# Kernel tuning notes

Hardware: AMD Instinct MI355X
Metric: run time of the kernel (lower is better)

## Reference

```python
import jax, jax.numpy as jnp
import numpy as np

B, S, E = 4, 4096, 1024
H = 16
D = E // H            # per-head dim (k_dim == v_dim == 64)
N_SAMPLE = 1024       # tokens kept per (batch, head)


def setup_inputs() -> dict:
    key = jax.random.key(0)
    ks = jax.random.split(key, 7)
    lim = float(np.sqrt(6.0 / (E + E)))  # xavier_uniform for square weight
    x = jax.random.normal(ks[0], (B, S, E), dtype=jnp.float32)
    Wq = jax.random.uniform(ks[1], (E, E), jnp.float32, -lim, lim)
    Wk = jax.random.uniform(ks[2], (E, E), jnp.float32, -lim, lim)
    Wv = jax.random.uniform(ks[3], (E, E), jnp.float32, -lim, lim)
    bq = jnp.zeros((E,), jnp.float32)
    bk = jnp.zeros((E,), jnp.float32)
    bv = jnp.zeros((E,), jnp.float32)
    return {"x": x, "Wq": Wq, "bq": bq, "Wk": Wk, "bk": bk, "Wv": Wv, "bv": bv}


def reference(x, Wq, bq, Wk, bk, Wv, bv):
    Bs, Sl, Ed = x.shape
    # projections -> [B, H, S, D]
    q = (x @ Wq.T + bq).reshape(Bs, Sl, H, D).transpose(0, 2, 1, 3)
    k = (x @ Wk.T + bk).reshape(Bs, Sl, H, D).transpose(0, 2, 1, 3)
    v = (x @ Wv.T + bv).reshape(Bs, Sl, H, D).transpose(0, 2, 1, 3)

    # cosFormer feature map: relu + cos/sin positional reweighting
    pos = jnp.arange(Sl, dtype=x.dtype)
    theta = (jnp.pi / 2.0) * pos / Sl            # [S]
    cos_w = jnp.cos(theta)[None, None, :, None]  # [1,1,S,1]
    sin_w = jnp.sin(theta)[None, None, :, None]
    qn = jax.nn.relu(q)
    kn = jax.nn.relu(k)
    q_cos, q_sin = qn * cos_w, qn * sin_w
    k_cos, k_sin = kn * cos_w, kn * sin_w

    # token sampler: top-N_SAMPLE tokens by (q*k).sum(-1) per (b,h)
    scores = jnp.sum(q * k, axis=-1)             # [B,H,S]
    _, idx = jax.lax.top_k(scores, N_SAMPLE)     # [B,H,n]

    # global K^T V reductions: [B,H,D,D]
    kv_cos = jnp.einsum("bhsd,bhse->bhde", k_cos, v)
    kv_sin = jnp.einsum("bhsd,bhse->bhde", k_sin, v)

    # gather sampled queries: [B,H,n,D]
    qs_cos = jnp.take_along_axis(q_cos, idx[..., None], axis=2)
    qs_sin = jnp.take_along_axis(q_sin, idx[..., None], axis=2)

    sampled = (jnp.einsum("bhnd,bhde->bhne", qs_cos, kv_cos)
               + jnp.einsum("bhnd,bhde->bhne", qs_sin, kv_sin))  # [B,H,n,D]

    # scatter-add back into zeros at sampled positions
    bi = jnp.arange(Bs)[:, None, None]
    hi = jnp.arange(H)[None, :, None]
    values = jnp.zeros((Bs, H, Sl, D), sampled.dtype).at[bi, hi, idx].add(sampled)

    out = values.transpose(0, 2, 1, 3).reshape(Bs, Sl, H * D)
    return out  # o_proj is Identity (v_dim*num_heads == embed_dim); dropout=0
```

## Files before the change

### kernel.cpp

```cpp
#include <hip/hip_runtime.h>
#include <hip/hip_bf16.h>

#define B_ 4
#define S_ 4096
#define E_ 1024
#define H_ 16
#define D_ 64
#define NS_ 1024
#define M_ (B_*S_)
#define K_ E_
#define DELTA 0.12f
#define BANDCAP 96

typedef __attribute__((ext_vector_type(8))) short bf16x8;
typedef __attribute__((ext_vector_type(4))) float floatx4;

#define THSTEP 0.00038349519697141023f

__device__ inline float bf16_to_f(unsigned short u) {
    return __uint_as_float(((unsigned)u) << 16);
}
__device__ inline unsigned short f_to_bf16(float f) {
    unsigned u = __float_as_uint(f);
    unsigned r = (u + 0x7FFFu + ((u >> 16) & 1u)) >> 16;
    return (unsigned short)r;
}

__device__ inline void gl_lds16(const void* g, void* l) {
    __builtin_amdgcn_global_load_lds(
        (const __attribute__((address_space(1))) void*)g,
        (__attribute__((address_space(3))) void*)l, 16, 0, 0);
}

__global__ __launch_bounds__(256) void split_x_kernel(
    const float* __restrict__ x, ushort* __restrict__ xh)
{
    int i = blockIdx.x * 256 + threadIdx.x;
    float4 v = ((const float4*)x)[i];
    ushort4 hh;
    hh.x = f_to_bf16(v.x); hh.y = f_to_bf16(v.y);
    hh.z = f_to_bf16(v.z); hh.w = f_to_bf16(v.w);
    ((ushort4*)xh)[i] = hh;
}

__global__ __launch_bounds__(256) void split_w_kernel(
    const float* __restrict__ Wq, const float* __restrict__ Wk,
    const float* __restrict__ Wv,
    ushort* __restrict__ Wqh, ushort* __restrict__ Wql,
    ushort* __restrict__ Wkh, ushort* __restrict__ Wkl,
    ushort* __restrict__ Wvh)
{
    int i = blockIdx.x * 256 + threadIdx.x;
    float4 q = ((const float4*)Wq)[i];
    float4 k = ((const float4*)Wk)[i];
    float4 v = ((const float4*)Wv)[i];
    ushort4 h, l;
    h.x=f_to_bf16(q.x); l.x=f_to_bf16(q.x-bf16_to_f(h.x));
    h.y=f_to_bf16(q.y); l.y=f_to_bf16(q.y-bf16_to_f(h.y));
    h.z=f_to_bf16(q.z); l.z=f_to_bf16(q.z-bf16_to_f(h.z));
    h.w=f_to_bf16(q.w); l.w=f_to_bf16(q.w-bf16_to_f(h.w));
    ((ushort4*)Wqh)[i]=h; ((ushort4*)Wql)[i]=l;
    h.x=f_to_bf16(k.x); l.x=f_to_bf16(k.x-bf16_to_f(h.x));
    h.y=f_to_bf16(k.y); l.y=f_to_bf16(k.y-bf16_to_f(h.y));
    h.z=f_to_bf16(k.z); l.z=f_to_bf16(k.z-bf16_to_f(h.z));
    h.w=f_to_bf16(k.w); l.w=f_to_bf16(k.w-bf16_to_f(h.w));
    ((ushort4*)Wkh)[i]=h; ((ushort4*)Wkl)[i]=l;
    h.x=f_to_bf16(v.x); h.y=f_to_bf16(v.y);
    h.z=f_to_bf16(v.z); h.w=f_to_bf16(v.w);
    ((ushort4*)Wvh)[i]=h;
}

__global__ __launch_bounds__(256) void qkv_gemm(
    const ushort* __restrict__ xh,
    const ushort* __restrict__ Wqh, const ushort* __restrict__ Wql,
    const ushort* __restrict__ Wkh, const ushort* __restrict__ Wkl,
    const ushort* __restrict__ Wvh,
    const float* __restrict__ bq, const float* __restrict__ bk,
    const float* __restrict__ bv,
    float* __restrict__ q32, float* __restrict__ k32, ushort* __restrict__ v16)
{
    __shared__ __align__(16) ushort As[128 * 64];
    __shared__ __align__(16) ushort Bsh[128 * 64];
    __shared__ __align__(16) ushort Bsl[128 * 64];

    const int w = blockIdx.z;
    const ushort* Bhp = (w == 0) ? Wqh : (w == 1) ? Wkh : Wvh;
    const ushort* Blp = (w == 0) ? Wql : Wkl;
    const float* bias = (w == 0) ? bq : (w == 1) ? bk : bv;
    const bool lo = (w < 2);

    const int m0 = blockIdx.x * 128;
    const int n0 = blockIdx.y * 128;
    const int t = threadIdx.x;
    const int wave = t >> 6, lane = t & 63;
    const int wm = (wave >> 1) * 64, wn = (wave & 1) * 64;
    const int m16 = lane & 15, quad = lane >> 4;

    floatx4 acc[4][4];
#pragma unroll
    for (int i = 0; i < 4; i++)
#pragma unroll
        for (int j = 0; j < 4; j++) acc[i][j] = (floatx4){0.f, 0.f, 0.f, 0.f};

    int aoff[4], boff[4], lbase[4];
#pragma unroll
    for (int i = 0; i < 4; i++) {
        int slot = i * 256 + t;
        int r = slot >> 3, c = slot & 7, g = c ^ (r & 7);
        aoff[i] = (m0 + r) * K_ + g * 8;
        boff[i] = (n0 + r) * K_ + g * 8;
        lbase[i] = (i * 256 + wave * 64) * 8;
    }

    for (int ks = 0; ks < 16; ++ks) {
        const int kcol = ks * 64;
#pragma unroll
        for (int i = 0; i < 4; i++) {
            gl_lds16(xh + aoff[i] + kcol, &As[lbase[i]]);
            gl_lds16(Bhp + boff[i] + kcol, &Bsh[lbase[i]]);
        }
        if (lo) {
#pragma unroll
            for (int i = 0; i < 4; i++)
                gl_lds16(Blp + boff[i] + kcol, &Bsl[lbase[i]]);
        }
        __syncthreads();

#pragma unroll
        for (int kk = 0; kk < 2; ++kk) {
            bf16x8 af[4], bfr[4];
            const int g = kk * 4 + quad;
#pragma unroll
            for (int mt = 0; mt < 4; ++mt) {
                int r = wm + mt * 16 + m16;
                af[mt] = *(const bf16x8*)&As[(r * 8 + (g ^ (r & 7))) * 8];
            }
#pragma unroll
            for (int nt = 0; nt < 4; ++nt) {
                int r2 = wn + nt * 16 + m16;
                bfr[nt] = *(const bf16x8*)&Bsh[(r2 * 8 + (g ^ (r2 & 7))) * 8];
            }
#pragma unroll
            for (int mt = 0; mt < 4; ++mt)
#pragma unroll
                for (int nt = 0; nt < 4; ++nt)
                    acc[mt][nt] = __builtin_amdgcn_mfma_f32_16x16x32_bf16(
                        af[mt], bfr[nt], acc[mt][nt], 0, 0, 0);
            if (lo) {
#pragma unroll
                for (int nt = 0; nt < 4; ++nt) {
                    int r2 = wn + nt * 16 + m16;
                    bfr[nt] = *(const bf16x8*)&Bsl[(r2 * 8 + (g ^ (r2 & 7))) * 8];
                }
#pragma unroll
                for (int mt = 0; mt < 4; ++mt)
#pragma unroll
                    for (int nt = 0; nt < 4; ++nt)
                        acc[mt][nt] = __builtin_amdgcn_mfma_f32_16x16x32_bf16(
                            af[mt], bfr[nt], acc[mt][nt], 0, 0, 0);
            }
        }
        __syncthreads();
    }

    float biasv[4];
#pragma unroll
    for (int nt = 0; nt < 4; nt++)
        biasv[nt] = bias[n0 + wn + nt * 16 + m16];

    if (w < 2) {
        float* dst = (w == 0) ? q32 : k32;
#pragma unroll
        for (int mt = 0; mt < 4; ++mt)
#pragma unroll
            for (int nt = 0; nt < 4; ++nt) {
                int colg = n0 + wn + nt * 16 + m16;
#pragma unroll
                for (int reg = 0; reg < 4; ++reg) {
                    int rowg = m0 + wm + mt * 16 + quad * 4 + reg;
                    dst[(size_t)rowg * E_ + colg] = acc[mt][nt][reg] + biasv[nt];
                }
            }
    } else {
#pragma unroll
        for (int mt = 0; mt < 4; ++mt)
#pragma unroll
            for (int nt = 0; nt < 4; ++nt) {
                int colg = n0 + wn + nt * 16 + m16;
#pragma unroll
                for (int reg = 0; reg < 4; ++reg) {
                    int rowg = m0 + wm + mt * 16 + quad * 4 + reg;
                    v16[(size_t)rowg * E_ + colg] = f_to_bf16(acc[mt][nt][reg] + biasv[nt]);
                }
            }
    }
}

__global__ __launch_bounds__(256) void scores_kernel(
    const float* __restrict__ q32, const float* __restrict__ k32,
    float* __restrict__ scores)
{
    int wid = blockIdx.x * 4 + (threadIdx.x >> 6);
    int lane = threadIdx.x & 63;
    int s = wid & (S_ - 1);
    int bh = wid >> 12;
    int b = bh >> 4, h = bh & 15;
    size_t addr = (size_t)(b * S_ + s) * E_ + h * 64 + lane;
    float p = q32[addr] * k32[addr];
#pragma unroll
    for (int m = 32; m; m >>= 1) p += __shfl_xor(p, m, 64);
    if (lane == 0) scores[wid] = p;
}

__global__ __launch_bounds__(256) void band_select_kernel(
    const float* __restrict__ scores, int* __restrict__ selidx,
    int* __restrict__ band, int* __restrict__ meta)
{
    __shared__ unsigned keys[4096];
    __shared__ unsigned hist[256];
    __shared__ unsigned suf[256];
    __shared__ unsigned bcast[2];
    __shared__ int cnt_in, cnt_band;

    int bh = blockIdx.x;
    int t = threadIdx.x;
    const float* sc = scores + (size_t)bh * S_;

    for (int i = t; i < 4096; i += 256) {
        unsigned u = __float_as_uint(sc[i]);
        u = (u & 0x80000000u) ? ~u : (u | 0x80000000u);
        keys[i] = u;
    }
    if (t == 0) { cnt_in = 0; cnt_band = 0; }
    __syncthreads();

    unsigned prefix = 0, want = NS_;
    for (int shift = 24; shift >= 0; shift -= 8) {
        hist[t] = 0;
        __syncthreads();
        unsigned pmask = (shift == 24) ? 0u : (0xFFFFFFFFu << (shift + 8));
        for (int i = t; i < 4096; i += 256) {
            unsigned ky = keys[i];
            if ((ky & pmask) == prefix) atomicAdd(&hist[(ky >> shift) & 255u], 1u);
        }
        __syncthreads();
        suf[t] = hist[t];
        __syncthreads();
        for (int off = 1; off < 256; off <<= 1) {
            unsigned add = (t + off < 256) ? suf[t + off] : 0u;
            __syncthreads();
            suf[t] += add;
            __syncthreads();
        }
        unsigned Sb = suf[t];
        unsigned Snx = (t < 255) ? suf[t + 1] : 0u;
        if (Sb >= want && Snx < want) {
            bcast[0] = (unsigned)t;
            bcast[1] = want - Snx;
        }
        __syncthreads();
        prefix = prefix | (bcast[0] << shift);
        want = bcast[1];
        __syncthreads();
    }
    unsigned fb = (prefix & 0x80000000u) ? (prefix ^ 0x80000000u) : ~prefix;
    float Ta = __uint_as_float(fb);
    float Thi = Ta + DELTA, Tlo = Ta - DELTA;

    int* sel = selidx + (size_t)bh * NS_;
    int* bnd = band + (size_t)bh * BANDCAP;
    for (int i = t; i < 4096; i += 256) {
        float v = sc[i];
        if (v > Thi) {
            int p = atomicAdd(&cnt_in, 1);
            sel[p] = i;
        } else if (v >= Tlo) {
            int p = atomicAdd(&cnt_band, 1);
            if (p < BANDCAP) bnd[p] = i;
        }
    }
    __syncthreads();
    if (t == 0) {
        meta[bh * 2 + 0] = cnt_in;
        meta[bh * 2 + 1] = (cnt_band < BANDCAP) ? cnt_band : BANDCAP;
    }
}

__global__ __launch_bounds__(512) void band_exact_kernel(
    const float* __restrict__ x,
    const float* __restrict__ Wq, const float* __restrict__ Wk,
    const int* __restrict__ band, const int* __restrict__ meta,
    double* __restrict__ bscore)
{
    int j = blockIdx.x, bh = blockIdx.y;
    int NB = meta[bh * 2 + 1];
    if (j >= NB) return;
    int b = bh >> 4, h = bh & 15;
    int s = band[(size_t)bh * BANDCAP + j];
    int t = threadIdx.x;
    int wave = t >> 6, lane = t & 63;

    __shared__ float xs[1024];
    __shared__ double qkd[128];

    if (t < 256)
        *(float4*)&xs[t * 4] = *(const float4*)(x + (size_t)(b * S_ + s) * K_ + t * 4);
    __syncthreads();

    const float* Wbase = (wave < 4) ? Wq : Wk;
    int role = wave >> 2;
    int dbase = (wave & 3) * 16;
    const float4* xs4 = (const float4*)xs;

    for (int rr = 0; rr < 16; ++rr) {
        int d = dbase + rr;
        const float4* wrow4 = (const float4*)(Wbase + (size_t)(h * 64 + d) * K_);
        double a = 0.0;
#pragma unroll
        for (int p = 0; p < 4; ++p) {
            float4 wv = wrow4[lane + 64 * p];
            float4 xv = xs4[lane + 64 * p];
            a += (double)xv.x * wv.x + (double)xv.y * wv.y
               + (double)xv.z * wv.z + (double)xv.w * wv.w;
        }
#pragma unroll
        for (int m = 32; m; m >>= 1) a += __shfl_xor(a, m, 64);
        if (lane == 0) qkd[role * 64 + d] = a;
    }
    __syncthreads();

    if (t < 64) {
        double p = qkd[t] * qkd[64 + t];
#pragma unroll
        for (int m = 32; m; m >>= 1) p += __shfl_xor(p, m, 64);
        if (t == 0) bscore[(size_t)bh * BANDCAP + j] = p;
    }
}

__global__ __launch_bounds__(128) void band_rank_kernel(
    const double* __restrict__ bscore, const int* __restrict__ band,
    const int* __restrict__ meta, int* __restrict__ selidx)
{
    __shared__ double sc[BANDCAP];
    __shared__ int bi[BANDCAP];
    int bh = blockIdx.x, t = threadIdx.x;
    int cnt_in = meta[bh * 2 + 0], NB = meta[bh * 2 + 1];
    int need = NS_ - cnt_in;
    if (t < NB) {
        sc[t] = bscore[(size_t)bh * BANDCAP + t];
        bi[t] = band[(size_t)bh * BANDCAP + t];
    }
    __syncthreads();
    if (t < NB) {
        double mine = sc[t]; int myi = bi[t]; int r = 0;
        for (int j2 = 0; j2 < NB; ++j2)
            r += (sc[j2] > mine) || (sc[j2] == mine && bi[j2] < myi);
        if (r < need) selidx[(size_t)bh * NS_ + cnt_in + r] = myi;
    }
}

__global__ __launch_bounds__(256) void kv_partial_kernel(
    const float* __restrict__ k32, const ushort* __restrict__ v16,
    float* __restrict__ kvp)
{
    __shared__ float kls[16 * 64];
    __shared__ float vls[16 * 64];
    int ch = blockIdx.x;
    int bh = blockIdx.y;
    int b = bh >> 4, h = bh & 15;
    int t = threadIdx.x;
    int d0 = (t >> 4) * 4, e0 = (t & 15) * 4;
    int lr = t >> 4, lc = (t & 15) * 4;

    float accC[4][4] = {}, accS[4][4] = {};
    const float* kbase = k32 + (size_t)b * S_ * E_ + h * 64;
    const ushort* vbase = v16 + (size_t)b * S_ * E_ + h * 64;
    int s0 = ch * 256;

    for (int g = 0; g < 16; ++g) {
        int srow = s0 + g * 16 + lr;
        float4 kf = *(const float4*)(kbase + (size_t)srow * E_ + lc);
        ushort4 vu = *(const ushort4*)(vbase + (size_t)srow * E_ + lc);
        __syncthreads();
        *(float4*)&kls[lr * 64 + lc] = kf;
        float4 vf = { bf16_to_f(vu.x), bf16_to_f(vu.y),
                      bf16_to_f(vu.z), bf16_to_f(vu.w) };
        *(float4*)&vls[lr * 64 + lc] = vf;
        __syncthreads();
#pragma unroll 4
        for (int si = 0; si < 16; ++si) {
            int s = s0 + g * 16 + si;
            float th = (float)s * THSTEP;
            float cw = __cosf(th), sw = __sinf(th);
            float4 kf2 = *(const float4*)&kls[si * 64 + d0];
            float4 vf2 = *(const float4*)&vls[si * 64 + e0];
            float kr[4] = { fmaxf(kf2.x, 0.f), fmaxf(kf2.y, 0.f),
                            fmaxf(kf2.z, 0.f), fmaxf(kf2.w, 0.f) };
            float vv[4] = { vf2.x, vf2.y, vf2.z, vf2.w };
            float kc[4], ksn[4];
#pragma unroll
            for (int i = 0; i < 4; i++) { kc[i] = kr[i] * cw; ksn[i] = kr[i] * sw; }
#pragma unroll
            for (int i = 0; i < 4; i++)
#pragma unroll
                for (int jj = 0; jj < 4; jj++) {
                    accC[i][jj] += kc[i] * vv[jj];
                    accS[i][jj] += ksn[i] * vv[jj];
                }
        }
    }
    float* pc = kvp + ((size_t)(bh * 16 + ch) * 2) * 4096;
    float* ps = pc + 4096;
#pragma unroll
    for (int i = 0; i < 4; i++)
#pragma unroll
        for (int jj = 0; jj < 4; jj++) {
            pc[(d0 + i) * 64 + (e0 + jj)] = accC[i][jj];
            ps[(d0 + i) * 64 + (e0 + jj)] = accS[i][jj];
        }
}

__global__ __launch_bounds__(256) void kv_reduce_kernel(
    const float* __restrict__ kvp, float* __restrict__ kv)
{
    int i = blockIdx.x * 256 + threadIdx.x;
    if (i >= 64 * 2 * 4096) return;
    int bh = i >> 13;
    int rem = i & 8191;
    const float* p = kvp + (size_t)bh * 16 * 8192 + rem;
    float a = 0.f;
#pragma unroll
    for (int c = 0; c < 16; c++) a += p[c * 8192];
    kv[i] = a;
}

__global__ __launch_bounds__(256) void sampled_kernel(
    const float* __restrict__ q32, const int* __restrict__ selidx,
    const float* __restrict__ kv, float* __restrict__ out)
{
    __shared__ float kvc[4096];
    __shared__ float kvs[4096];
    __shared__ float qs[256 * 65];
    __shared__ int sidx[256];
    int bh = blockIdx.y;
    int b = bh >> 4, h = bh & 15;
    int t = threadIdx.x;
    int wave = t >> 6, lane = t & 63;

    const float* kvsrc = kv + (size_t)bh * 8192;
    for (int i = t; i < 4096; i += 256) {
        kvc[i] = kvsrc[i];
        kvs[i] = kvsrc[4096 + i];
    }
    sidx[t] = selidx[(size_t)bh * NS_ + blockIdx.x * 256 + t];
    __syncthreads();

    for (int i = 0; i < 64; ++i) {
        int row = wave * 64 + i;
        int sr = sidx[row];
        qs[row * 65 + lane] = q32[(size_t)(b * S_ + sr) * E_ + h * 64 + lane];
    }
    __syncthreads();

    int s = sidx[t];
    float th = (float)s * THSTEP;
    float cw = __cosf(th), sw = __sinf(th);

    float acc[64];
#pragma unroll
    for (int e = 0; e < 64; e++) acc[e] = 0.f;

    for (int d = 0; d < 64; ++d) {
        float qd = fmaxf(qs[t * 65 + d], 0.f);
        float a = qd * cw, bb = qd * sw;
        const float4* pc4 = (const float4*)&kvc[d * 64];
        const float4* ps4 = (const float4*)&kvs[d * 64];
#pragma unroll
        for (int e4 = 0; e4 < 16; e4++) {
            float4 c4 = pc4[e4], s4 = ps4[e4];
            acc[e4 * 4 + 0] += a * c4.x + bb * s4.x;
            acc[e4 * 4 + 1] += a * c4.y + bb * s4.y;
            acc[e4 * 4 + 2] += a * c4.z + bb * s4.z;
            acc[e4 * 4 + 3] += a * c4.w + bb * s4.w;
        }
    }
    __syncthreads();
#pragma unroll
    for (int e = 0; e < 64; e++) qs[t * 65 + e] = acc[e];
    __syncthreads();

    for (int i = 0; i < 64; ++i) {
        int row = wave * 64 + i;
        int sr = sidx[row];
        out[(size_t)(b * S_ + sr) * E_ + h * 64 + lane] = qs[row * 65 + lane];
    }
}

__global__ void zero_kernel(uint4* __restrict__ p, int n16)
{
    int stride = gridDim.x * blockDim.x;
    for (int i = blockIdx.x * blockDim.x + threadIdx.x; i < n16; i += stride)
        p[i] = make_uint4(0u, 0u, 0u, 0u);
}

extern "C" void kernel_launch(void* const* d_in, const int* in_sizes, int n_in,
                              void* d_out, int out_size, void* d_ws, size_t ws_size,
                              hipStream_t stream)
{
    const float* x  = (const float*)d_in[0];
    const float* Wq = (const float*)d_in[1];
    const float* bq = (const float*)d_in[2];
    const float* Wk = (const float*)d_in[3];
    const float* bk = (const float*)d_in[4];
    const float* Wv = (const float*)d_in[5];
    const float* bv = (const float*)d_in[6];

    char* ws = (char*)d_ws;
    ushort* xh     = (ushort*)(ws);
    float*  kvp    = (float*)(ws);
    float*  q32    = (float*)(ws + 33554432);
    float*  k32    = (float*)(ws + 100663296);
    ushort* v16    = (ushort*)(ws + 167772160);
    ushort* Wqh    = (ushort*)(ws + 201326592);
    ushort* Wql    = (ushort*)(ws + 203423744);
    ushort* Wkh    = (ushort*)(ws + 205520896);
    ushort* Wkl    = (ushort*)(ws + 207618048);
    ushort* Wvh    = (ushort*)(ws + 209715200);
    float*  scores = (float*)(ws + 211812352);
    int*    selidx = (int*)(ws + 212860928);
    int*    band   = (int*)(ws + 213123072);
    double* bscore = (double*)(ws + 213147648);
    int*    meta   = (int*)(ws + 213196800);
    float*  kv     = (float*)(ws + 213197312);
    float*  out    = (float*)d_out;

    hipLaunchKernelGGL(zero_kernel, dim3(2048), dim3(256), 0, stream,
                       (uint4*)out, (int)((size_t)M_ * E_ * 4 / 16));
    hipLaunchKernelGGL(split_x_kernel, dim3((M_ * K_) / 1024), dim3(256), 0, stream,
                       x, xh);
    hipLaunchKernelGGL(split_w_kernel, dim3((E_ * E_) / 1024), dim3(256), 0, stream,
                       Wq, Wk, Wv, Wqh, Wql, Wkh, Wkl, Wvh);
    hipLaunchKernelGGL(qkv_gemm, dim3(128, 8, 3), dim3(256), 0, stream,
                       xh, Wqh, Wql, Wkh, Wkl, Wvh, bq, bk, bv, q32, k32, v16);
    hipLaunchKernelGGL(scores_kernel, dim3((B_ * H_ * S_) / 4), dim3(256), 0, stream,
                       q32, k32, scores);
    hipLaunchKernelGGL(band_select_kernel, dim3(B_ * H_), dim3(256), 0, stream,
                       scores, selidx, band, meta);
    hipLaunchKernelGGL(band_exact_kernel, dim3(BANDCAP, B_ * H_), dim3(512), 0, stream,
                       x, Wq, Wk, band, meta, bscore);
    hipLaunchKernelGGL(band_rank_kernel, dim3(B_ * H_), dim3(128), 0, stream,
                       bscore, band, meta, selidx);
    hipLaunchKernelGGL(kv_partial_kernel, dim3(16, 64), dim3(256), 0, stream,
                       k32, v16, kvp);
    hipLaunchKernelGGL(kv_reduce_kernel, dim3(2048), dim3(256), 0, stream,
                       kvp, kv);
    hipLaunchKernelGGL(sampled_kernel, dim3(NS_ / 256, B_ * H_), dim3(256), 0, stream,
                       q32, selidx, kv, out);
}
```

Before: 550.0 us.

## Vectorize scores, packed-FMA kv partials, split-accumulator band dot, retile sampled kernel

The scores kernel now uses 16 threads per token with float4 loads instead of a full wave with scalar loads. kv_partial accumulates into 2-wide float vectors so the compiler can emit packed FP32 FMAs. band_exact splits its double-precision accumulation into four independent chains. sampled_kernel is retiled to 64 tokens per block with 4 threads per token, which cuts the 64-float accumulator array and LDS footprint and uses vectorized gathers and stores. These changes target memory efficiency and occupancy in the smaller kernels, and they slightly change the order of floating-point accumulation.

```diff
diff --git a/kernel.cpp b/kernel.cpp
--- a/kernel.cpp
+++ b/kernel.cpp
@@ -14,6 +14,7 @@
 
 typedef __attribute__((ext_vector_type(8))) short bf16x8;
 typedef __attribute__((ext_vector_type(4))) float floatx4;
+typedef __attribute__((ext_vector_type(2))) float f32x2;
 
 #define THSTEP 0.00038349519697141023f
 
@@ -200,16 +201,18 @@
     const float* __restrict__ q32, const float* __restrict__ k32,
     float* __restrict__ scores)
 {
-    int wid = blockIdx.x * 4 + (threadIdx.x >> 6);
-    int lane = threadIdx.x & 63;
-    int s = wid & (S_ - 1);
-    int bh = wid >> 12;
+    int g = blockIdx.x * 16 + (threadIdx.x >> 4);
+    int sub = threadIdx.x & 15;
+    int s = g & (S_ - 1);
+    int bh = g >> 12;
     int b = bh >> 4, h = bh & 15;
-    size_t addr = (size_t)(b * S_ + s) * E_ + h * 64 + lane;
-    float p = q32[addr] * k32[addr];
-#pragma unroll
-    for (int m = 32; m; m >>= 1) p += __shfl_xor(p, m, 64);
-    if (lane == 0) scores[wid] = p;
+    size_t addr = (size_t)(b * S_ + s) * E_ + h * 64 + sub * 4;
+    float4 qv = *(const float4*)(q32 + addr);
+    float4 kv = *(const float4*)(k32 + addr);
+    float p = qv.x * kv.x + qv.y * kv.y + qv.z * kv.z + qv.w * kv.w;
+#pragma unroll
+    for (int m = 8; m; m >>= 1) p += __shfl_xor(p, m, 64);
+    if (sub == 0) scores[g] = p;
 }
 
 __global__ __launch_bounds__(256) void band_select_kernel(
@@ -315,14 +318,17 @@
     for (int rr = 0; rr < 16; ++rr) {
         int d = dbase + rr;
         const float4* wrow4 = (const float4*)(Wbase + (size_t)(h * 64 + d) * K_);
-        double a = 0.0;
+        double a0 = 0.0, a1 = 0.0, a2 = 0.0, a3 = 0.0;
 #pragma unroll
         for (int p = 0; p < 4; ++p) {
             float4 wv = wrow4[lane + 64 * p];
             float4 xv = xs4[lane + 64 * p];
-            a += (double)xv.x * wv.x + (double)xv.y * wv.y
-               + (double)xv.z * wv.z + (double)xv.w * wv.w;
-        }
+            a0 += (double)xv.x * wv.x;
+            a1 += (double)xv.y * wv.y;
+            a2 += (double)xv.z * wv.z;
+            a3 += (double)xv.w * wv.w;
+        }
+        double a = (a0 + a1) + (a2 + a3);
 #pragma unroll
         for (int m = 32; m; m >>= 1) a += __shfl_xor(a, m, 64);
         if (lane == 0) qkd[role * 64 + d] = a;
@@ -372,7 +378,7 @@
     int d0 = (t >> 4) * 4, e0 = (t & 15) * 4;
     int lr = t >> 4, lc = (t & 15) * 4;
 
-    float accC[4][4] = {}, accS[4][4] = {};
+    f32x2 accC[4][2] = {}, accS[4][2] = {};
     const float* kbase = k32 + (size_t)b * S_ * E_ + h * 64;
     const ushort* vbase = v16 + (size_t)b * S_ * E_ + h * 64;
     int s0 = ch * 256;
@@ -396,28 +402,29 @@
             float4 vf2 = *(const float4*)&vls[si * 64 + e0];
             float kr[4] = { fmaxf(kf2.x, 0.f), fmaxf(kf2.y, 0.f),
                             fmaxf(kf2.z, 0.f), fmaxf(kf2.w, 0.f) };
-            float vv[4] = { vf2.x, vf2.y, vf2.z, vf2.w };
-            float kc[4], ksn[4];
-#pragma unroll
-            for (int i = 0; i < 4; i++) { kc[i] = kr[i] * cw; ksn[i] = kr[i] * sw; }
-#pragma unroll
-            for (int i = 0; i < 4; i++)
-#pragma unroll
-                for (int jj = 0; jj < 4; jj++) {
-                    accC[i][jj] += kc[i] * vv[jj];
-                    accS[i][jj] += ksn[i] * vv[jj];
-                }
+            f32x2 v01 = { vf2.x, vf2.y }, v23 = { vf2.z, vf2.w };
+#pragma unroll
+            for (int i = 0; i < 4; i++) {
+                f32x2 kc2 = { kr[i] * cw, kr[i] * cw };
+                f32x2 ks2 = { kr[i] * sw, kr[i] * sw };
+                accC[i][0] += kc2 * v01;  accC[i][1] += kc2 * v23;
+                accS[i][0] += ks2 * v01;  accS[i][1] += ks2 * v23;
+            }
         }
     }
     float* pc = kvp + ((size_t)(bh * 16 + ch) * 2) * 4096;
     float* ps = pc + 4096;
 #pragma unroll
-    for (int i = 0; i < 4; i++)
-#pragma unroll
-        for (int jj = 0; jj < 4; jj++) {
-            pc[(d0 + i) * 64 + (e0 + jj)] = accC[i][jj];
-            ps[(d0 + i) * 64 + (e0 + jj)] = accS[i][jj];
-        }
+    for (int i = 0; i < 4; i++) {
+        pc[(d0 + i) * 64 + e0 + 0] = accC[i][0][0];
+        pc[(d0 + i) * 64 + e0 + 1] = accC[i][0][1];
+        pc[(d0 + i) * 64 + e0 + 2] = accC[i][1][0];
+        pc[(d0 + i) * 64 + e0 + 3] = accC[i][1][1];
+        ps[(d0 + i) * 64 + e0 + 0] = accS[i][0][0];
+        ps[(d0 + i) * 64 + e0 + 1] = accS[i][0][1];
+        ps[(d0 + i) * 64 + e0 + 2] = accS[i][1][0];
+        ps[(d0 + i) * 64 + e0 + 3] = accS[i][1][1];
+    }
 }
 
 __global__ __launch_bounds__(256) void kv_reduce_kernel(
@@ -438,61 +445,67 @@
     const float* __restrict__ q32, const int* __restrict__ selidx,
     const float* __restrict__ kv, float* __restrict__ out)
 {
-    __shared__ float kvc[4096];
-    __shared__ float kvs[4096];
-    __shared__ float qs[256 * 65];
-    __shared__ int sidx[256];
+    __shared__ __align__(16) float kvc[4096];
+    __shared__ __align__(16) float kvs[4096];
+    __shared__ __align__(16) float qs[64 * 68];
+    __shared__ int sidx[64];
     int bh = blockIdx.y;
     int b = bh >> 4, h = bh & 15;
     int t = threadIdx.x;
-    int wave = t >> 6, lane = t & 63;
-
-    const float* kvsrc = kv + (size_t)bh * 8192;
-    for (int i = t; i < 4096; i += 256) {
-        kvc[i] = kvsrc[i];
-        kvs[i] = kvsrc[4096 + i];
-    }
-    sidx[t] = selidx[(size_t)bh * NS_ + blockIdx.x * 256 + t];
-    __syncthreads();
-
-    for (int i = 0; i < 64; ++i) {
-        int row = wave * 64 + i;
+
+    const float4* kvsrc4 = (const float4*)(kv + (size_t)bh * 8192);
+    float4* kvc4 = (float4*)kvc;
+    float4* kvs4 = (float4*)kvs;
+#pragma unroll
+    for (int i = 0; i < 4; ++i) {
+        kvc4[i * 256 + t] = kvsrc4[i * 256 + t];
+        kvs4[i * 256 + t] = kvsrc4[1024 + i * 256 + t];
+    }
+    if (t < 64) sidx[t] = selidx[(size_t)bh * NS_ + blockIdx.x * 64 + t];
+    __syncthreads();
+
+#pragma unroll
+    for (int c = 0; c < 4; ++c) {
+        int i = c * 256 + t;
+        int row = i >> 4, qp = i & 15;
         int sr = sidx[row];
-        qs[row * 65 + lane] = q32[(size_t)(b * S_ + sr) * E_ + h * 64 + lane];
-    }
-    __syncthreads();
-
-    int s = sidx[t];
-    float th = (float)s * THSTEP;
+        *(float4*)&qs[row * 68 + qp * 4] =
+            *(const float4*)(q32 + (size_t)(b * S_ + sr) * E_ + h * 64 + qp * 4);
+    }
+    __syncthreads();
+
+    int tok = t >> 2, eq = t & 3;
+    int sr = sidx[tok];
+    float th = (float)sr * THSTEP;
     float cw = __cosf(th), sw = __sinf(th);
 
-    float acc[64];
-#pragma unroll
-    for (int e = 0; e < 64; e++) acc[e] = 0.f;
-
+    f32x2 acc2[8];
+#pragma unroll
+    for (int e = 0; e < 8; e++) acc2[e] = (f32x2){0.f, 0.f};
+
+    const float4* kvcb = (const float4*)&kvc[eq * 16];
+    const float4* kvsb = (const float4*)&kvs[eq * 16];
     for (int d = 0; d < 64; ++d) {
-        float qd = fmaxf(qs[t * 65 + d], 0.f);
-        float a = qd * cw, bb = qd * sw;
-        const float4* pc4 = (const float4*)&kvc[d * 64];
-        const float4* ps4 = (const float4*)&kvs[d * 64];
-#pragma unroll
-        for (int e4 = 0; e4 < 16; e4++) {
-            float4 c4 = pc4[e4], s4 = ps4[e4];
-            acc[e4 * 4 + 0] += a * c4.x + bb * s4.x;
-            acc[e4 * 4 + 1] += a * c4.y + bb * s4.y;
-            acc[e4 * 4 + 2] += a * c4.z + bb * s4.z;
-            acc[e4 * 4 + 3] += a * c4.w + bb * s4.w;
-        }
-    }
-    __syncthreads();
-#pragma unroll
-    for (int e = 0; e < 64; e++) qs[t * 65 + e] = acc[e];
-    __syncthreads();
-
-    for (int i = 0; i < 64; ++i) {
-        int row = wave * 64 + i;
-        int sr = sidx[row];
-        out[(size_t)(b * S_ + sr) * E_ + h * 64 + lane] = qs[row * 65 + lane];
+        float qd = fmaxf(qs[tok * 68 + d], 0.f);
+        f32x2 a2 = { qd * cw, qd * cw };
+        f32x2 b2 = { qd * sw, qd * sw };
+#pragma unroll
+        for (int c = 0; c < 4; ++c) {
+            float4 c4 = kvcb[d * 16 + c];
+            float4 s4 = kvsb[d * 16 + c];
+            f32x2 c01 = { c4.x, c4.y }, c23 = { c4.z, c4.w };
+            f32x2 s01 = { s4.x, s4.y }, s23 = { s4.z, s4.w };
+            acc2[c * 2 + 0] += a2 * c01 + b2 * s01;
+            acc2[c * 2 + 1] += a2 * c23 + b2 * s23;
+        }
+    }
+
+    float* dst = out + (size_t)(b * S_ + sr) * E_ + h * 64 + eq * 16;
+#pragma unroll
+    for (int c = 0; c < 4; ++c) {
+        float4 o = { acc2[c * 2 + 0][0], acc2[c * 2 + 0][1],
+                     acc2[c * 2 + 1][0], acc2[c * 2 + 1][1] };
+        *(float4*)(dst + c * 4) = o;
     }
 }
 
@@ -542,7 +555,7 @@
                        Wq, Wk, Wv, Wqh, Wql, Wkh, Wkl, Wvh);
     hipLaunchKernelGGL(qkv_gemm, dim3(128, 8, 3), dim3(256), 0, stream,
                        xh, Wqh, Wql, Wkh, Wkl, Wvh, bq, bk, bv, q32, k32, v16);
-    hipLaunchKernelGGL(scores_kernel, dim3((B_ * H_ * S_) / 4), dim3(256), 0, stream,
+    hipLaunchKernelGGL(scores_kernel, dim3((B_ * H_ * S_) / 16), dim3(256), 0, stream,
                        q32, k32, scores);
     hipLaunchKernelGGL(band_select_kernel, dim3(B_ * H_), dim3(256), 0, stream,
                        scores, selidx, band, meta);
@@ -554,6 +567,6 @@
                        k32, v16, kvp);
     hipLaunchKernelGGL(kv_reduce_kernel, dim3(2048), dim3(256), 0, stream,
                        kvp, kv);
-    hipLaunchKernelGGL(sampled_kernel, dim3(NS_ / 256, B_ * H_), dim3(256), 0, stream,
+    hipLaunchKernelGGL(sampled_kernel, dim3(NS_ / 64, B_ * H_), dim3(256), 0, stream,
                        q32, selidx, kv, out);
 }
```

New measurement: 562.4 us. 1.02x slower.
